# Optimization experiments

Hardware: AMD Instinct MI355X
Metric: run time of the kernel (lower is better)

Reference implementation:

```python
import jax, jax.numpy as jnp
import numpy as np

K_SIZE = 3
STRIDE = 1
PAD = 1
DIL = 1


def conv2d(x, w, b):
    # standard dense conv, NCHW / OIHW, stride 1, symmetric padding
    y = jax.lax.conv_general_dilated(
        x, w, window_strides=(1, 1), padding=[(PAD, PAD), (PAD, PAD)],
        dimension_numbers=("NCHW", "OIHW", "NCHW"))
    return y + b[None, :, None, None]


def deform_conv2d(x, offset, mask, w):
    """Modulated deformable conv (DCNv2), groups=1, deformable_groups=1, no bias.
    x: [B,C,H,W], offset: [B,2*K,H,W] (dy,dx per tap), mask: [B,K,H,W], w: [O,C,k,k].
    """
    B, C, H, W = x.shape
    k = K_SIZE
    K = k * k
    Ho, Wo = H, W  # stride 1, pad 1, dil 1, k 3 -> same spatial size
    off = offset.reshape(B, K, 2, Ho, Wo)
    dy, dx = off[:, :, 0], off[:, :, 1]
    # integer sampling grid per kernel tap
    ky = (jnp.arange(K) // k).astype(x.dtype) * DIL  # tap row offset
    kx = (jnp.arange(K) % k).astype(x.dtype) * DIL   # tap col offset
    gy = jnp.arange(Ho, dtype=x.dtype) * STRIDE - PAD
    gx = jnp.arange(Wo, dtype=x.dtype) * STRIDE - PAD
    py = gy[None, :, None] + ky[:, None, None] + dy  # [B,K,Ho,Wo]
    px = gx[None, None, :] + kx[:, None, None] + dx  # [B,K,Ho,Wo]

    y0 = jnp.floor(py)
    x0 = jnp.floor(px)
    wy1 = py - y0  # frac weights
    wx1 = px - x0
    y0i = y0.astype(jnp.int32)
    x0i = x0.astype(jnp.int32)

    x_flat = x.reshape(B, C, H * W)

    def corner(yi, xi, wgt):
        # zero-padded bilinear corner: out-of-bounds contributes 0
        valid = (yi >= 0) & (yi < H) & (xi >= 0) & (xi < W)
        idx = (jnp.clip(yi, 0, H - 1) * W + jnp.clip(xi, 0, W - 1)).reshape(B, 1, K * Ho * Wo)
        v = jnp.take_along_axis(x_flat, idx, axis=2)  # [B,C,K*Ho*Wo]
        return v * (wgt * valid.astype(x.dtype)).reshape(B, 1, K * Ho * Wo)

    cols = (corner(y0i, x0i, (1 - wy1) * (1 - wx1))
            + corner(y0i, x0i + 1, (1 - wy1) * wx1)
            + corner(y0i + 1, x0i, wy1 * (1 - wx1))
            + corner(y0i + 1, x0i + 1, wy1 * wx1))
    cols = cols * mask.reshape(B, 1, K * Ho * Wo)          # modulation
    cols = cols.reshape(B, C, K, Ho, Wo)
    return jnp.einsum("bckhw,ock->bohw", cols, w.reshape(w.shape[0], C, K))


def setup_inputs() -> dict:
    key = jax.random.key(0)
    ks = jax.random.split(key, 4)
    B, C, H, W = 8, 64, 128, 128
    O = 64
    k = K_SIZE
    x = jax.random.normal(ks[0], (B, C, H, W), dtype=jnp.float32)
    # offset/mask generators are zero-init in the original; use small random weights
    # so the gather pattern is actually exercised while offsets stay near-grid.
    w_off = jax.random.normal(ks[1], (2 * k * k, C, k, k), dtype=jnp.float32) * 0.01
    b_off = jnp.zeros((2 * k * k,), dtype=jnp.float32)
    w_mask = jax.random.normal(ks[2], (k * k, C, k, k), dtype=jnp.float32) * 0.01
    b_mask = jnp.zeros((k * k,), dtype=jnp.float32)
    w_dcn = jax.random.normal(ks[3], (O, C, k, k), dtype=jnp.float32) * 0.059  # He init std
    return {"x": x, "w_off": w_off, "b_off": b_off, "w_mask": w_mask, "b_mask": b_mask, "w_dcn": w_dcn}


def reference(x, w_off, b_off, w_mask, b_mask, w_dcn):
    offset = conv2d(x, w_off, b_off)
    mask = jax.nn.sigmoid(conv2d(x, w_mask, b_mask))
    return deform_conv2d(x, offset, mask, w_dcn)
```

## Files before the change

kernel.cpp:

```cpp
#include <hip/hip_runtime.h>
#include <hip/hip_bf16.h>
#include <math.h>

#define BB 8
#define CC 64
#define HH 128
#define WW 128
#define OO 64
#define HWHW (HH*WW)

typedef short bf16x8 __attribute__((ext_vector_type(8)));
typedef float f32x4 __attribute__((ext_vector_type(4)));
typedef unsigned short ushort_t;
typedef unsigned int uint32;

__device__ __forceinline__ float bflo(uint32 u) {
  return __builtin_bit_cast(float, u << 16);
}
__device__ __forceinline__ float bfhi(uint32 u) {
  return __builtin_bit_cast(float, u & 0xffff0000u);
}
__device__ __forceinline__ ushort_t f2bf(float f) {
  __hip_bfloat16 h = __float2bfloat16(f);
  return *(ushort_t*)&h;
}

__global__ __launch_bounds__(256) void k_transpose(const float* __restrict__ x,
                                                   ushort_t* __restrict__ xt) {
  __shared__ float tile[64][65];
  int blk = blockIdx.x;
  int b = blk >> 8;
  int hw0 = (blk & 255) << 6;
  int lane = threadIdx.x & 63;
  int g = threadIdx.x >> 6;
  const float* xb = x + (size_t)b * CC * HWHW;
#pragma unroll
  for (int i = 0; i < 16; ++i) {
    int c = g + i * 4;
    tile[lane][c] = xb[c * HWHW + hw0 + lane];
  }
  __syncthreads();
  ushort_t* xtb = xt + (size_t)b * HWHW * 64;
#pragma unroll
  for (int j = 0; j < 16; ++j) {
    int hwl = g + j * 4;
    xtb[(size_t)(hw0 + hwl) * 64 + lane] = f2bf(tile[hwl][lane]);
  }
}

__global__ __launch_bounds__(256) void k_wcast(const float* __restrict__ w_dcn,
                                               const float* __restrict__ w_off,
                                               const float* __restrict__ w_mask,
                                               ushort_t* __restrict__ wbf,
                                               ushort_t* __restrict__ w_om) {
  int i = blockIdx.x * 256 + threadIdx.x;
  if (i < 36864) {
    int o = i / 576;
    int ck = i % 576;
    int c = ck / 9;
    int t = ck % 9;
    wbf[o * 576 + t * 64 + c] = f2bf(w_dcn[i]);
  } else {
    int j = i - 36864;
    int o = j / 576;
    int r = j % 576;
    int t = r / 64;
    int c = r % 64;
    float v = 0.f;
    if (o < 18) v = w_off[o * 576 + c * 9 + t];
    else if (o < 27) v = w_mask[(o - 18) * 576 + c * 9 + t];
    w_om[j] = f2bf(v);
  }
}

#define HALO_OFF 0
#define TAPW_OFF 17280
#define TAPA_OFF 22032
#define OFFM_OFF 26784
#define FB_OFF   31392
#define RED_OFF  0
#define FB_MAX   16
#define SM_TOTAL 31680
__global__ __launch_bounds__(256, 5) void k_deform(const ushort_t* __restrict__ xtbf,
                                                   const ushort_t* __restrict__ w_om,
                                                   const float* __restrict__ b_off,
                                                   const float* __restrict__ b_mask,
                                                   const ushort_t* __restrict__ wbf,
                                                   float* __restrict__ out) {
  __shared__ __align__(16) unsigned char smem[SM_TOTAL];
  float* offm = (float*)(smem + OFFM_OFF);
  f32x4* red = (f32x4*)(smem + RED_OFF);

  int bi = blockIdx.x;
  int b = bi & 7;
  int idx = bi >> 3;
  int y = (idx >> 3) * 2;
  int x0 = (idx & 7) * 16;
  int tid = threadIdx.x;
  int wave = tid >> 6;
  int lane = tid & 63;
  int mr = lane & 15;
  int kg = lane >> 4;
  int pr = wave >> 1;
  const ushort_t* xbu = xtbf + (size_t)b * HWHW * 64;
  const char* xb8 = (const char*)xbu;

  if (tid == 0) *(int*)(smem + FB_OFF) = 0;
  {
    int c8 = (tid & 15) * 8;
#pragma unroll
    for (int i = 0; i < 8; ++i) {
      int pos = (tid >> 4) + i * 16;
      if (pos < 120) {
        int r = pos / 20;
        int j = pos - r * 20;
        int yy = y - 2 + r;
        int xx = x0 - 2 + j;
        uint2 d = make_uint2(0u, 0u);
        if (((unsigned)yy < (unsigned)HH) && ((unsigned)xx < (unsigned)WW))
          d = *(const uint2*)(xb8 + ((size_t)(yy * WW + xx) << 7) + c8);
        *(uint2*)(smem + pos * 144 + c8) = d;
      }
    }
  }
  __syncthreads();

  {
    int ot = wave & 1;
    f32x4 cacc = {0.f, 0.f, 0.f, 0.f};
    const ushort_t* wrow = w_om + (size_t)(ot * 16 + mr) * 576 + kg * 8;
#pragma unroll
    for (int s = 0; s < 18; ++s) {
      int t = s >> 1, h = s & 1;
      int ky = t / 3, kx = t % 3;
      int pos = (pr + ky + 1) * 20 + (mr + kx + 1);
      bf16x8 a = *(const bf16x8*)(smem + pos * 144 + h * 64 + kg * 16);
      bf16x8 bb = *(const bf16x8*)(wrow + s * 32);
      cacc = __builtin_amdgcn_mfma_f32_16x16x32_bf16(a, bb, cacc, 0, 0, 0);
    }
    int o = ot * 16 + mr;
    float bias = 0.f;
    if (o < 18) bias = b_off[o];
    else if (o < 27) bias = b_mask[o - 18];
    bool is_mask = (o >= 18) && (o < 27);
#pragma unroll
    for (int r = 0; r < 4; ++r) {
      float v = cacc[r] + bias;
      float sg = 1.f / (1.f + expf(-v));
      cacc[r] = is_mask ? sg : v;
    }
    *(f32x4*)&offm[o * 36 + pr * 16 + kg * 4] = cacc;
  }
  __syncthreads();

#pragma unroll
  for (int pass = 0; pass < 2; ++pass) {
    int tau = tid + pass * 256;
    if (tau < 288) {
      int p = tau / 9;
      int k = tau - p * 9;
      float dy = offm[(2 * k) * 36 + p];
      float dx = offm[(2 * k + 1) * 36 + p];
      float m = offm[(18 + k) * 36 + p];
      int yy_o = y + (p >> 4);
      int xx_o = x0 + (p & 15);
      float py = (float)(yy_o + k / 3 - 1) + dy;
      float pxf = (float)(xx_o + k % 3 - 1) + dx;
      float fy = floorf(py), fx = floorf(pxf);
      int y0i = (int)fy, x0i = (int)fx;
      float wy1 = py - fy, wx1 = pxf - fx;
      float wyv[2] = {1.f - wy1, wy1};
      float wxv[2] = {1.f - wx1, wx1};
      uint32 wq[4], aq[4];
#pragma unroll
      for (int ry = 0; ry < 2; ++ry) {
#pragma unroll
        for (int rx = 0; rx < 2; ++rx) {
          int yiq = y0i + ry;
          int xiq = x0i + rx;
          float valid = (((unsigned)yiq < (unsigned)HH) &&
                         ((unsigned)xiq < (unsigned)WW)) ? 1.f : 0.f;
          int yc = min(max(yiq, 0), HH - 1);
          int xc = min(max(xiq, 0), WW - 1);
          int rr = yc - (y - 2);
          int jj = xc - (x0 - 2);
          float w = wyv[ry] * wxv[rx] * valid * m;
          int e = ry * 2 + rx;
          if ((unsigned)rr < 6u && (unsigned)jj < 20u) {
            aq[e] = (uint32)((rr * 20 + jj) * 144);
            wq[e] = __builtin_bit_cast(uint32, w);
          } else {
            int rrc = min(max(rr, 0), 5), jjc = min(max(jj, 0), 19);
            aq[e] = (uint32)((rrc * 20 + jjc) * 144);
            wq[e] = 0u;
            if (w != 0.f) {
              int slot = atomicAdd((int*)(smem + FB_OFF), 1);
              if (slot < FB_MAX) {
                *(uint4*)(smem + FB_OFF + 16 + slot * 16) =
                    make_uint4((uint32)p | ((uint32)k << 8),
                               (uint32)(yc * WW + xc),
                               __builtin_bit_cast(uint32, w), 0u);
              }
            }
          }
        }
      }
      *(uint4*)(smem + TAPW_OFF + (k * 33 + p) * 16) = make_uint4(wq[0], wq[1], wq[2], wq[3]);
      *(uint4*)(smem + TAPA_OFF + (k * 33 + p) * 16) = make_uint4(aq[0], aq[1], aq[2], aq[3]);
    }
  }
  __syncthreads();

  f32x4 acc0 = {0.f, 0.f, 0.f, 0.f}, acc1 = acc0, acc2 = acc0, acc3 = acc0;
  int fbn = min(*(const int*)(smem + FB_OFF), FB_MAX);
  fbn = __builtin_amdgcn_readfirstlane(fbn);
  {
    int kh = wave & 1;
    int px = pr * 16 + mr;
    int cb = kh * 64 + kg * 16;
    const ushort_t* wbase = wbf + (size_t)mr * 576 + kh * 32 + kg * 8;

    uint4 wqA, aqA, wqB, aqB, wqC, aqC;
    uint4 dA_0, dA_1, dA_2, dA_3, dB_0, dB_1, dB_2, dB_3;

#define TLOADX(S, I) {                                                        \
    wq##S = *(const uint4*)(smem + TAPW_OFF + ((I) * 33 + px) * 16);          \
    aq##S = *(const uint4*)(smem + TAPA_OFF + ((I) * 33 + px) * 16); }
#define CLOADX(BUF, S) {                                                      \
    d##BUF##_0 = *(const uint4*)(smem + aq##S.x + cb);                        \
    d##BUF##_1 = *(const uint4*)(smem + aq##S.y + cb);                        \
    d##BUF##_2 = *(const uint4*)(smem + aq##S.z + cb);                        \
    d##BUF##_3 = *(const uint4*)(smem + aq##S.w + cb); }
#define GSTEPX(S, BUF, T) {                                                   \
    float fw0 = __builtin_bit_cast(float, wq##S.x);                           \
    float fw1 = __builtin_bit_cast(float, wq##S.y);                           \
    float fw2 = __builtin_bit_cast(float, wq##S.z);                           \
    float fw3 = __builtin_bit_cast(float, wq##S.w);                           \
    float s0 = fw0 * bflo(d##BUF##_0.x), s1 = fw0 * bfhi(d##BUF##_0.x);       \
    float s2 = fw0 * bflo(d##BUF##_0.y), s3 = fw0 * bfhi(d##BUF##_0.y);       \
    float s4 = fw0 * bflo(d##BUF##_0.z), s5 = fw0 * bfhi(d##BUF##_0.z);       \
    float s6 = fw0 * bflo(d##BUF##_0.w), s7 = fw0 * bfhi(d##BUF##_0.w);       \
    s0 += fw1 * bflo(d##BUF##_1.x); s1 += fw1 * bfhi(d##BUF##_1.x);           \
    s2 += fw1 * bflo(d##BUF##_1.y); s3 += fw1 * bfhi(d##BUF##_1.y);           \
    s4 += fw1 * bflo(d##BUF##_1.z); s5 += fw1 * bfhi(d##BUF##_1.z);           \
    s6 += fw1 * bflo(d##BUF##_1.w); s7 += fw1 * bfhi(d##BUF##_1.w);           \
    s0 += fw2 * bflo(d##BUF##_2.x); s1 += fw2 * bfhi(d##BUF##_2.x);           \
    s2 += fw2 * bflo(d##BUF##_2.y); s3 += fw2 * bfhi(d##BUF##_2.y);           \
    s4 += fw2 * bflo(d##BUF##_2.z); s5 += fw2 * bfhi(d##BUF##_2.z);           \
    s6 += fw2 * bflo(d##BUF##_2.w); s7 += fw2 * bfhi(d##BUF##_2.w);           \
    s0 += fw3 * bflo(d##BUF##_3.x); s1 += fw3 * bfhi(d##BUF##_3.x);           \
    s2 += fw3 * bflo(d##BUF##_3.y); s3 += fw3 * bfhi(d##BUF##_3.y);           \
    s4 += fw3 * bflo(d##BUF##_3.z); s5 += fw3 * bfhi(d##BUF##_3.z);           \
    s6 += fw3 * bflo(d##BUF##_3.w); s7 += fw3 * bfhi(d##BUF##_3.w);           \
    if (fbn) {                                \
      for (int e = 0; e < fbn; ++e) {                                         \
        uint4 ent = *(const uint4*)(smem + FB_OFF + 16 + e * 16);             \
        if ((int)(ent.x >> 8) == (T) && (int)(ent.x & 255u) == px) {          \
          uint4 d = *(const uint4*)(xb8 + ((size_t)ent.y << 7) + cb);         \
          float fw = __builtin_bit_cast(float, ent.z);                        \
          s0 += fw * bflo(d.x); s1 += fw * bfhi(d.x);                         \
          s2 += fw * bflo(d.y); s3 += fw * bfhi(d.y);                         \
          s4 += fw * bflo(d.z); s5 += fw * bfhi(d.z);                         \
          s6 += fw * bflo(d.w); s7 += fw * bfhi(d.w);                         \
        }                                                                     \
      }                                                                       \
    }                                                                         \
    uint32 p0 = __builtin_amdgcn_perm(__builtin_bit_cast(uint32, s1) + 0x8000u, \
                                      __builtin_bit_cast(uint32, s0) + 0x8000u, \
                                      0x07060302u);                           \
    uint32 p1 = __builtin_amdgcn_perm(__builtin_bit_cast(uint32, s3) + 0x8000u, \
                                      __builtin_bit_cast(uint32, s2) + 0x8000u, \
                                      0x07060302u);                           \
    uint32 p2 = __builtin_amdgcn_perm(__builtin_bit_cast(uint32, s5) + 0x8000u, \
                                      __builtin_bit_cast(uint32, s4) + 0x8000u, \
                                      0x07060302u);                           \
    uint32 p3 = __builtin_amdgcn_perm(__builtin_bit_cast(uint32, s7) + 0x8000u, \
                                      __builtin_bit_cast(uint32, s6) + 0x8000u, \
                                      0x07060302u);                           \
    bf16x8 afrag = __builtin_bit_cast(bf16x8, make_uint4(p0, p1, p2, p3));    \
    const ushort_t* wp = wbase + (T) * 64;                                    \
    acc0 = __builtin_amdgcn_mfma_f32_16x16x32_bf16(afrag, *(const bf16x8*)(wp), acc0, 0, 0, 0); \
    acc1 = __builtin_amdgcn_mfma_f32_16x16x32_bf16(afrag, *(const bf16x8*)(wp + 9216), acc1, 0, 0, 0); \
    acc2 = __builtin_amdgcn_mfma_f32_16x16x32_bf16(afrag, *(const bf16x8*)(wp + 18432), acc2, 0, 0, 0); \
    acc3 = __builtin_amdgcn_mfma_f32_16x16x32_bf16(afrag, *(const bf16x8*)(wp + 27648), acc3, 0, 0, 0); }

    TLOADX(A, 0) TLOADX(B, 1) CLOADX(A, A)
    TLOADX(C, 2) CLOADX(B, B) GSTEPX(A, A, 0)
    TLOADX(A, 3) CLOADX(A, C) GSTEPX(B, B, 1)
    TLOADX(B, 4) CLOADX(B, A) GSTEPX(C, A, 2)
    TLOADX(C, 5) CLOADX(A, B) GSTEPX(A, B, 3)
    TLOADX(A, 6) CLOADX(B, C) GSTEPX(B, A, 4)
    TLOADX(B, 7) CLOADX(A, A) GSTEPX(C, B, 5)
    TLOADX(C, 8) CLOADX(B, B) GSTEPX(A, A, 6)
                 CLOADX(A, C) GSTEPX(B, B, 7)
                              GSTEPX(C, A, 8)
#undef TLOADX
#undef CLOADX
#undef GSTEPX
  }

  __syncthreads();
  {
    int kh = wave & 1;
    if (kh == 1) {
      red[(pr * 4 + 0) * 64 + lane] = acc0;
      red[(pr * 4 + 1) * 64 + lane] = acc1;
      red[(pr * 4 + 2) * 64 + lane] = acc2;
      red[(pr * 4 + 3) * 64 + lane] = acc3;
    }
    __syncthreads();
    if (kh == 0) {
      f32x4 v0 = acc0 + red[(pr * 4 + 0) * 64 + lane];
      f32x4 v1 = acc1 + red[(pr * 4 + 1) * 64 + lane];
      f32x4 v2 = acc2 + red[(pr * 4 + 2) * 64 + lane];
      f32x4 v3 = acc3 + red[(pr * 4 + 3) * 64 + lane];
      size_t rowoff = (size_t)(y + pr) * WW + x0 + kg * 4;
      *(f32x4*)(out + (size_t)(b * 64 + 0 * 16 + mr) * HWHW + rowoff) = v0;
      *(f32x4*)(out + (size_t)(b * 64 + 1 * 16 + mr) * HWHW + rowoff) = v1;
      *(f32x4*)(out + (size_t)(b * 64 + 2 * 16 + mr) * HWHW + rowoff) = v2;
      *(f32x4*)(out + (size_t)(b * 64 + 3 * 16 + mr) * HWHW + rowoff) = v3;
    }
  }
}

extern "C" void kernel_launch(void* const* d_in, const int* in_sizes, int n_in,
                              void* d_out, int out_size, void* d_ws, size_t ws_size,
                              hipStream_t stream) {
  const float* x = (const float*)d_in[0];
  const float* w_off = (const float*)d_in[1];
  const float* b_off = (const float*)d_in[2];
  const float* w_mask = (const float*)d_in[3];
  const float* b_mask = (const float*)d_in[4];
  const float* w_dcn = (const float*)d_in[5];
  float* out = (float*)d_out;

  char* ws = (char*)d_ws;
  ushort_t* xtbf = (ushort_t*)ws;
  ushort_t* wbf = (ushort_t*)(ws + 16777216);
  ushort_t* w_om = (ushort_t*)(ws + 16777216 + 73728);

  hipLaunchKernelGGL(k_transpose, dim3(2048), dim3(256), 0, stream, x, xtbf);
  hipLaunchKernelGGL(k_wcast, dim3(216), dim3(256), 0, stream, w_dcn, w_off, w_mask,
                     wbf, w_om);
  hipLaunchKernelGGL(k_deform, dim3(4096), dim3(256), 0, stream, xtbf, w_om,
                     b_off, b_mask, wbf, out);
}
```

Before: 131.2 us.

## Compute bilinear tap addresses and weights in gather loop instead of staging in LDS

Removes the per-tap weight and address tables in shared memory. Each lane now recomputes the bilinear corner addresses and weights directly from a transposed offset/mask tile that it holds in registers. Out-of-halo fallback samples are moved out of the per-tap inner loop into a separate pass with extra MFMAs after the main gather. Shared memory shrinks, but launch bounds drop from 5 to 4 blocks per SM and the gather loop does more ALU work and uses more registers.

New measurement: 123.0 us. -6.3%, faster.

```diff
diff --git a/kernel.cpp b/kernel.cpp
--- a/kernel.cpp
+++ b/kernel.cpp
@@ -23,6 +23,15 @@
 __device__ __forceinline__ ushort_t f2bf(float f) {
   __hip_bfloat16 h = __float2bfloat16(f);
   return *(ushort_t*)&h;
+}
+__device__ __forceinline__ int haddr(int rr, int jj, int cb) {
+  int rrc = min(max(rr, 0), 5);
+  int jjc = min(max(jj, 0), 19);
+  return rrc * 2880 + jjc * 144 + cb;
+}
+__device__ __forceinline__ float hwt(int rr, int jj, float wb, float m) {
+  bool inh = ((unsigned)rr < 6u) && ((unsigned)jj < 20u);
+  return inh ? wb * m : 0.f;
 }
 
 __global__ __launch_bounds__(256) void k_transpose(const float* __restrict__ x,
@@ -74,21 +83,19 @@
 }
 
 #define HALO_OFF 0
-#define TAPW_OFF 17280
-#define TAPA_OFF 22032
-#define OFFM_OFF 26784
-#define FB_OFF   31392
+#define OFFT_OFF 17280
+#define FB_OFF   22912
 #define RED_OFF  0
 #define FB_MAX   16
-#define SM_TOTAL 31680
-__global__ __launch_bounds__(256, 5) void k_deform(const ushort_t* __restrict__ xtbf,
+#define SM_TOTAL 23184
+__global__ __launch_bounds__(256, 4) void k_deform(const ushort_t* __restrict__ xtbf,
                                                    const ushort_t* __restrict__ w_om,
                                                    const float* __restrict__ b_off,
                                                    const float* __restrict__ b_mask,
                                                    const ushort_t* __restrict__ wbf,
                                                    float* __restrict__ out) {
   __shared__ __align__(16) unsigned char smem[SM_TOTAL];
-  float* offm = (float*)(smem + OFFM_OFF);
+  float* offt = (float*)(smem + OFFT_OFF);
   f32x4* red = (f32x4*)(smem + RED_OFF);
 
   int bi = blockIdx.x;
@@ -147,9 +154,9 @@
     for (int r = 0; r < 4; ++r) {
       float v = cacc[r] + bias;
       float sg = 1.f / (1.f + expf(-v));
-      cacc[r] = is_mask ? sg : v;
-    }
-    *(f32x4*)&offm[o * 36 + pr * 16 + kg * 4] = cacc;
+      float res = is_mask ? sg : v;
+      offt[(pr * 16 + kg * 4 + r) * 44 + o] = res;
+    }
   }
   __syncthreads();
 
@@ -159,9 +166,10 @@
     if (tau < 288) {
       int p = tau / 9;
       int k = tau - p * 9;
-      float dy = offm[(2 * k) * 36 + p];
-      float dx = offm[(2 * k + 1) * 36 + p];
-      float m = offm[(18 + k) * 36 + p];
+      const float* op = offt + p * 44;
+      float dy = op[2 * k];
+      float dx = op[2 * k + 1];
+      float m = op[18 + k];
       int yy_o = y + (p >> 4);
       int xx_o = x0 + (p & 15);
       float py = (float)(yy_o + k / 3 - 1) + dy;
@@ -171,42 +179,30 @@
       float wy1 = py - fy, wx1 = pxf - fx;
       float wyv[2] = {1.f - wy1, wy1};
       float wxv[2] = {1.f - wx1, wx1};
-      uint32 wq[4], aq[4];
 #pragma unroll
       for (int ry = 0; ry < 2; ++ry) {
 #pragma unroll
         for (int rx = 0; rx < 2; ++rx) {
           int yiq = y0i + ry;
           int xiq = x0i + rx;
-          float valid = (((unsigned)yiq < (unsigned)HH) &&
-                         ((unsigned)xiq < (unsigned)WW)) ? 1.f : 0.f;
-          int yc = min(max(yiq, 0), HH - 1);
-          int xc = min(max(xiq, 0), WW - 1);
-          int rr = yc - (y - 2);
-          int jj = xc - (x0 - 2);
-          float w = wyv[ry] * wxv[rx] * valid * m;
-          int e = ry * 2 + rx;
-          if ((unsigned)rr < 6u && (unsigned)jj < 20u) {
-            aq[e] = (uint32)((rr * 20 + jj) * 144);
-            wq[e] = __builtin_bit_cast(uint32, w);
-          } else {
-            int rrc = min(max(rr, 0), 5), jjc = min(max(jj, 0), 19);
-            aq[e] = (uint32)((rrc * 20 + jjc) * 144);
-            wq[e] = 0u;
+          bool valid = ((unsigned)yiq < (unsigned)HH) && ((unsigned)xiq < (unsigned)WW);
+          int rr = yiq - (y - 2);
+          int jj = xiq - (x0 - 2);
+          bool inh = ((unsigned)rr < 6u) && ((unsigned)jj < 20u);
+          if (valid && !inh) {
+            float w = wyv[ry] * wxv[rx] * m;
             if (w != 0.f) {
               int slot = atomicAdd((int*)(smem + FB_OFF), 1);
               if (slot < FB_MAX) {
                 *(uint4*)(smem + FB_OFF + 16 + slot * 16) =
                     make_uint4((uint32)p | ((uint32)k << 8),
-                               (uint32)(yc * WW + xc),
+                               (uint32)(yiq * WW + xiq),
                                __builtin_bit_cast(uint32, w), 0u);
               }
             }
           }
         }
       }
-      *(uint4*)(smem + TAPW_OFF + (k * 33 + p) * 16) = make_uint4(wq[0], wq[1], wq[2], wq[3]);
-      *(uint4*)(smem + TAPA_OFF + (k * 33 + p) * 16) = make_uint4(aq[0], aq[1], aq[2], aq[3]);
     }
   }
   __syncthreads();
@@ -214,57 +210,65 @@
   f32x4 acc0 = {0.f, 0.f, 0.f, 0.f}, acc1 = acc0, acc2 = acc0, acc3 = acc0;
   int fbn = min(*(const int*)(smem + FB_OFF), FB_MAX);
   fbn = __builtin_amdgcn_readfirstlane(fbn);
+  int kh = wave & 1;
+  int px = pr * 16 + mr;
+  int cb = kh * 64 + kg * 16;
+  const ushort_t* wbase = wbf + (size_t)mr * 576 + kh * 32 + kg * 8;
   {
-    int kh = wave & 1;
-    int px = pr * 16 + mr;
-    int cb = kh * 64 + kg * 16;
-    const ushort_t* wbase = wbf + (size_t)mr * 576 + kh * 32 + kg * 8;
-
-    uint4 wqA, aqA, wqB, aqB, wqC, aqC;
+    f32x4 ofr[7];
+    const float* offp = offt + px * 44;
+#pragma unroll
+    for (int i = 0; i < 7; ++i) ofr[i] = *(const f32x4*)(offp + i * 4);
+
+    int ybase = y + pr;
+    int xbase = x0 + mr;
+    int ybm2 = y - 2, xbm2 = x0 - 2;
+
+    int4 aA, aB;
+    f32x4 wA, wB;
     uint4 dA_0, dA_1, dA_2, dA_3, dB_0, dB_1, dB_2, dB_3;
 
-#define TLOADX(S, I) {                                                        \
-    wq##S = *(const uint4*)(smem + TAPW_OFF + ((I) * 33 + px) * 16);          \
-    aq##S = *(const uint4*)(smem + TAPA_OFF + ((I) * 33 + px) * 16); }
-#define CLOADX(BUF, S) {                                                      \
-    d##BUF##_0 = *(const uint4*)(smem + aq##S.x + cb);                        \
-    d##BUF##_1 = *(const uint4*)(smem + aq##S.y + cb);                        \
-    d##BUF##_2 = *(const uint4*)(smem + aq##S.z + cb);                        \
-    d##BUF##_3 = *(const uint4*)(smem + aq##S.w + cb); }
-#define GSTEPX(S, BUF, T) {                                                   \
-    float fw0 = __builtin_bit_cast(float, wq##S.x);                           \
-    float fw1 = __builtin_bit_cast(float, wq##S.y);                           \
-    float fw2 = __builtin_bit_cast(float, wq##S.z);                           \
-    float fw3 = __builtin_bit_cast(float, wq##S.w);                           \
-    float s0 = fw0 * bflo(d##BUF##_0.x), s1 = fw0 * bfhi(d##BUF##_0.x);       \
-    float s2 = fw0 * bflo(d##BUF##_0.y), s3 = fw0 * bfhi(d##BUF##_0.y);       \
-    float s4 = fw0 * bflo(d##BUF##_0.z), s5 = fw0 * bfhi(d##BUF##_0.z);       \
-    float s6 = fw0 * bflo(d##BUF##_0.w), s7 = fw0 * bfhi(d##BUF##_0.w);       \
-    s0 += fw1 * bflo(d##BUF##_1.x); s1 += fw1 * bfhi(d##BUF##_1.x);           \
-    s2 += fw1 * bflo(d##BUF##_1.y); s3 += fw1 * bfhi(d##BUF##_1.y);           \
-    s4 += fw1 * bflo(d##BUF##_1.z); s5 += fw1 * bfhi(d##BUF##_1.z);           \
-    s6 += fw1 * bflo(d##BUF##_1.w); s7 += fw1 * bfhi(d##BUF##_1.w);           \
-    s0 += fw2 * bflo(d##BUF##_2.x); s1 += fw2 * bfhi(d##BUF##_2.x);           \
-    s2 += fw2 * bflo(d##BUF##_2.y); s3 += fw2 * bfhi(d##BUF##_2.y);           \
-    s4 += fw2 * bflo(d##BUF##_2.z); s5 += fw2 * bfhi(d##BUF##_2.z);           \
-    s6 += fw2 * bflo(d##BUF##_2.w); s7 += fw2 * bfhi(d##BUF##_2.w);           \
-    s0 += fw3 * bflo(d##BUF##_3.x); s1 += fw3 * bfhi(d##BUF##_3.x);           \
-    s2 += fw3 * bflo(d##BUF##_3.y); s3 += fw3 * bfhi(d##BUF##_3.y);           \
-    s4 += fw3 * bflo(d##BUF##_3.z); s5 += fw3 * bfhi(d##BUF##_3.z);           \
-    s6 += fw3 * bflo(d##BUF##_3.w); s7 += fw3 * bfhi(d##BUF##_3.w);           \
-    if (fbn) {                                \
-      for (int e = 0; e < fbn; ++e) {                                         \
-        uint4 ent = *(const uint4*)(smem + FB_OFF + 16 + e * 16);             \
-        if ((int)(ent.x >> 8) == (T) && (int)(ent.x & 255u) == px) {          \
-          uint4 d = *(const uint4*)(xb8 + ((size_t)ent.y << 7) + cb);         \
-          float fw = __builtin_bit_cast(float, ent.z);                        \
-          s0 += fw * bflo(d.x); s1 += fw * bfhi(d.x);                         \
-          s2 += fw * bflo(d.y); s3 += fw * bfhi(d.y);                         \
-          s4 += fw * bflo(d.z); s5 += fw * bfhi(d.z);                         \
-          s6 += fw * bflo(d.w); s7 += fw * bfhi(d.w);                         \
-        }                                                                     \
-      }                                                                       \
-    }                                                                         \
+#define AW(S, T) {                                                            \
+    float dy_ = ofr[(2*(T))>>2][(2*(T))&3];                                   \
+    float dx_ = ofr[(2*(T)+1)>>2][(2*(T)+1)&3];                               \
+    float mm_ = ofr[(18+(T))>>2][(18+(T))&3];                                 \
+    float py_ = (float)(ybase + (T)/3 - 1) + dy_;                             \
+    float pxx_ = (float)(xbase + (T)%3 - 1) + dx_;                            \
+    float fy_ = floorf(py_), fx_ = floorf(pxx_);                              \
+    float wy1_ = py_ - fy_, wx1_ = pxx_ - fx_;                                \
+    float wy0_ = 1.f - wy1_, wx0_ = 1.f - wx1_;                               \
+    int rr_ = (int)fy_ - ybm2, jj_ = (int)fx_ - xbm2;                         \
+    a##S.x = haddr(rr_,     jj_,     cb);                                     \
+    a##S.y = haddr(rr_,     jj_ + 1, cb);                                     \
+    a##S.z = haddr(rr_ + 1, jj_,     cb);                                     \
+    a##S.w = haddr(rr_ + 1, jj_ + 1, cb);                                     \
+    w##S[0] = hwt(rr_,     jj_,     wy0_ * wx0_, mm_);                        \
+    w##S[1] = hwt(rr_,     jj_ + 1, wy0_ * wx1_, mm_);                        \
+    w##S[2] = hwt(rr_ + 1, jj_,     wy1_ * wx0_, mm_);                        \
+    w##S[3] = hwt(rr_ + 1, jj_ + 1, wy1_ * wx1_, mm_); }
+#define LD(S) {                                                               \
+    d##S##_0 = *(const uint4*)(smem + a##S.x);                                \
+    d##S##_1 = *(const uint4*)(smem + a##S.y);                                \
+    d##S##_2 = *(const uint4*)(smem + a##S.z);                                \
+    d##S##_3 = *(const uint4*)(smem + a##S.w); }
+#define GS(S, T) {                                                            \
+    float fw0 = w##S[0], fw1 = w##S[1], fw2 = w##S[2], fw3 = w##S[3];         \
+    float s0 = fw0 * bflo(d##S##_0.x), s1 = fw0 * bfhi(d##S##_0.x);           \
+    float s2 = fw0 * bflo(d##S##_0.y), s3 = fw0 * bfhi(d##S##_0.y);           \
+    float s4 = fw0 * bflo(d##S##_0.z), s5 = fw0 * bfhi(d##S##_0.z);           \
+    float s6 = fw0 * bflo(d##S##_0.w), s7 = fw0 * bfhi(d##S##_0.w);           \
+    s0 += fw1 * bflo(d##S##_1.x); s1 += fw1 * bfhi(d##S##_1.x);               \
+    s2 += fw1 * bflo(d##S##_1.y); s3 += fw1 * bfhi(d##S##_1.y);               \
+    s4 += fw1 * bflo(d##S##_1.z); s5 += fw1 * bfhi(d##S##_1.z);               \
+    s6 += fw1 * bflo(d##S##_1.w); s7 += fw1 * bfhi(d##S##_1.w);               \
+    s0 += fw2 * bflo(d##S##_2.x); s1 += fw2 * bfhi(d##S##_2.x);               \
+    s2 += fw2 * bflo(d##S##_2.y); s3 += fw2 * bfhi(d##S##_2.y);               \
+    s4 += fw2 * bflo(d##S##_2.z); s5 += fw2 * bfhi(d##S##_2.z);               \
+    s6 += fw2 * bflo(d##S##_2.w); s7 += fw2 * bfhi(d##S##_2.w);               \
+    s0 += fw3 * bflo(d##S##_3.x); s1 += fw3 * bfhi(d##S##_3.x);               \
+    s2 += fw3 * bflo(d##S##_3.y); s3 += fw3 * bfhi(d##S##_3.y);               \
+    s4 += fw3 * bflo(d##S##_3.z); s5 += fw3 * bfhi(d##S##_3.z);               \
+    s6 += fw3 * bflo(d##S##_3.w); s7 += fw3 * bfhi(d##S##_3.w);               \
     uint32 p0 = __builtin_amdgcn_perm(__builtin_bit_cast(uint32, s1) + 0x8000u, \
                                       __builtin_bit_cast(uint32, s0) + 0x8000u, \
                                       0x07060302u);                           \
@@ -284,24 +288,57 @@
     acc2 = __builtin_amdgcn_mfma_f32_16x16x32_bf16(afrag, *(const bf16x8*)(wp + 18432), acc2, 0, 0, 0); \
     acc3 = __builtin_amdgcn_mfma_f32_16x16x32_bf16(afrag, *(const bf16x8*)(wp + 27648), acc3, 0, 0, 0); }
 
-    TLOADX(A, 0) TLOADX(B, 1) CLOADX(A, A)
-    TLOADX(C, 2) CLOADX(B, B) GSTEPX(A, A, 0)
-    TLOADX(A, 3) CLOADX(A, C) GSTEPX(B, B, 1)
-    TLOADX(B, 4) CLOADX(B, A) GSTEPX(C, A, 2)
-    TLOADX(C, 5) CLOADX(A, B) GSTEPX(A, B, 3)
-    TLOADX(A, 6) CLOADX(B, C) GSTEPX(B, A, 4)
-    TLOADX(B, 7) CLOADX(A, A) GSTEPX(C, B, 5)
-    TLOADX(C, 8) CLOADX(B, B) GSTEPX(A, A, 6)
-                 CLOADX(A, C) GSTEPX(B, B, 7)
-                              GSTEPX(C, A, 8)
-#undef TLOADX
-#undef CLOADX
-#undef GSTEPX
+    AW(A, 0) LD(A)
+    AW(B, 1) LD(B)
+    GS(A, 0) AW(A, 2) LD(A)
+    GS(B, 1) AW(B, 3) LD(B)
+    GS(A, 2) AW(A, 4) LD(A)
+    GS(B, 3) AW(B, 5) LD(B)
+    GS(A, 4) AW(A, 6) LD(A)
+    GS(B, 5) AW(B, 7) LD(B)
+    GS(A, 6) AW(A, 8) LD(A)
+    GS(B, 7)
+    GS(A, 8)
+#undef AW
+#undef LD
+#undef GS
+  }
+
+  if (fbn) {
+    for (int e = 0; e < fbn; ++e) {
+      uint4 ent = *(const uint4*)(smem + FB_OFF + 16 + e * 16);
+      int fpx = (int)(ent.x & 255u);
+      int ft = (int)(ent.x >> 8);
+      float fw = (mr == (fpx & 15) && pr == (fpx >> 4))
+                     ? __builtin_bit_cast(float, ent.z) : 0.f;
+      uint4 d = *(const uint4*)(xb8 + ((size_t)ent.y << 7) + cb);
+      float s0 = fw * bflo(d.x), s1 = fw * bfhi(d.x);
+      float s2 = fw * bflo(d.y), s3 = fw * bfhi(d.y);
+      float s4 = fw * bflo(d.z), s5 = fw * bfhi(d.z);
+      float s6 = fw * bflo(d.w), s7 = fw * bfhi(d.w);
+      uint32 p0 = __builtin_amdgcn_perm(__builtin_bit_cast(uint32, s1) + 0x8000u,
+                                        __builtin_bit_cast(uint32, s0) + 0x8000u,
+                                        0x07060302u);
+      uint32 p1 = __builtin_amdgcn_perm(__builtin_bit_cast(uint32, s3) + 0x8000u,
+                                        __builtin_bit_cast(uint32, s2) + 0x8000u,
+                                        0x07060302u);
+      uint32 p2 = __builtin_amdgcn_perm(__builtin_bit_cast(uint32, s5) + 0x8000u,
+                                        __builtin_bit_cast(uint32, s4) + 0x8000u,
+                                        0x07060302u);
+      uint32 p3 = __builtin_amdgcn_perm(__builtin_bit_cast(uint32, s7) + 0x8000u,
+                                        __builtin_bit_cast(uint32, s6) + 0x8000u,
+                                        0x07060302u);
+      bf16x8 afrag = __builtin_bit_cast(bf16x8, make_uint4(p0, p1, p2, p3));
+      const ushort_t* wp = wbase + ft * 64;
+      acc0 = __builtin_amdgcn_mfma_f32_16x16x32_bf16(afrag, *(const bf16x8*)(wp), acc0, 0, 0, 0);
+      acc1 = __builtin_amdgcn_mfma_f32_16x16x32_bf16(afrag, *(const bf16x8*)(wp + 9216), acc1, 0, 0, 0);
+      acc2 = __builtin_amdgcn_mfma_f32_16x16x32_bf16(afrag, *(const bf16x8*)(wp + 18432), acc2, 0, 0, 0);
+      acc3 = __builtin_amdgcn_mfma_f32_16x16x32_bf16(afrag, *(const bf16x8*)(wp + 27648), acc3, 0, 0, 0);
+    }
   }
 
   __syncthreads();
   {
-    int kh = wave & 1;
     if (kh == 1) {
       red[(pr * 4 + 0) * 64 + lane] = acc0;
       red[(pr * 4 + 1) * 64 + lane] = acc1;
```
